# Kernel optimization log

Hardware: AMD Instinct MI355X
Metric: run time of the kernel (lower is better)

The kernel has to match this reference:

```python
import jax, jax.numpy as jnp
import numpy as np

B, N = 4, 4096
SA = 128          # SA_conv_out
DGD = 1024        # DG_conv_out
EDC = 4           # ED_conv_out
CO = 128          # conv_out
FACTOR = 0.1      # ED_radius_factor


def setup_inputs() -> dict:
    key = jax.random.key(0)
    ks = iter(jax.random.split(key, 48))
    def w(shape, s=0.02):
        return jax.random.normal(next(ks), shape, jnp.float32) * s
    def bnp(c):
        # fused inference-mode batchnorm: scale = gamma/sqrt(var+eps), shift = beta - mean*scale
        return (1.0 + jax.random.normal(next(ks), (c,), jnp.float32) * 0.05,
                jax.random.normal(next(ks), (c,), jnp.float32) * 0.05)
    xyz = jax.random.normal(next(ks), (B, N, 3), jnp.float32)
    h1 = jax.random.normal(next(ks), (B, SA, N), jnp.float32)
    h2_in = jax.random.normal(next(ks), (B, DGD, N), jnp.float32)
    dg_s1, dg_t1 = bnp(256); dg_s2, dg_t2 = bnp(64); dg_s3, dg_t3 = bnp(SA // 4)
    s1, t1 = bnp(512); s2, t2 = bnp(256); s3, t3 = bnp(CO)
    return dict(
        xyz=xyz, h1=h1, h2_in=h2_in,
        dg_w1=w((256, DGD)), dg_b1=w((256,)), dg_s1=dg_s1, dg_t1=dg_t1,
        dg_w2=w((64, 256)), dg_b2=w((64,)), dg_s2=dg_s2, dg_t2=dg_t2,
        dg_w3=w((SA // 4, 64)), dg_b3=w((SA // 4,)), dg_s3=dg_s3, dg_t3=dg_t3,
        ed_w1=w((EDC, 3), 0.3), ed_b1=w((EDC,)), ed_w2=w((EDC, EDC), 0.3), ed_b2=w((EDC,)),
        w1=w((512, SA + SA // 4 + EDC)), b1=w((512,)), s1=s1, t1=t1,
        w2=w((256, 512)), b2=w((256,)), s2=s2, t2=t2,
        w3=w((CO, 256)), b3=w((CO,)), s3=s3, t3=t3,
    )


def _conv_bn_relu(x, W, b, s, t):
    # 1x1 Conv1d + inference BN + ReLU. x: [B, Cin, N]
    y = jnp.einsum('oc,pcn->pon', W, x) + b[:, None]
    return jax.nn.relu(y * s[:, None] + t[:, None])


def _eigen_features(xyz):
    # xyz: [B, N, 3]. Adaptive-radius neighbor mask, per-point covariance, eigvalsh.
    x2 = jnp.sum(xyz * xyz, axis=-1)                                   # [B, N]
    d2 = x2[:, :, None] + x2[:, None, :] - 2.0 * jnp.einsum('pia,pja->pij', xyz, xyz)
    d = jnp.sqrt(jnp.maximum(d2, 0.0))                                 # [B, N, N]
    radius = jnp.max(d, axis=(1, 2)) * FACTOR                          # max pairwise dist per cloud
    eye = jnp.eye(N, dtype=bool)
    mask = (d < radius[:, None, None]) & ~eye                          # [B, N, N] self excluded
    wf = mask.astype(xyz.dtype)
    cnt = jnp.sum(wf, axis=-1)                                         # [B, N]
    S1 = jnp.einsum('pij,pja->pia', wf, xyz)                           # sum of neighbors
    mu = S1 / jnp.maximum(cnt, 1.0)[..., None]                         # neighbor mean
    S2 = jnp.einsum('pij,pja,pjb->piab', wf, xyz, xyz)                 # [B, N, 3, 3]
    # original divides by neighbors_mask[i].shape[0] == N (total points)
    cov = (S2 - cnt[..., None, None] * mu[..., :, None] * mu[..., None, :]) / N
    return jnp.linalg.eigvalsh(cov)                                    # [B, N, 3]


def reference(xyz, h1, h2_in,
              dg_w1, dg_b1, dg_s1, dg_t1,
              dg_w2, dg_b2, dg_s2, dg_t2,
              dg_w3, dg_b3, dg_s3, dg_t3,
              ed_w1, ed_b1, ed_w2, ed_b2,
              w1, b1, s1, t1, w2, b2, s2, t2, w3, b3, s3, t3):
    # DG feature reduction 1024 -> 256 -> 64 -> 32
    h2 = _conv_bn_relu(h2_in, dg_w1, dg_b1, dg_s1, dg_t1)
    h2 = _conv_bn_relu(h2, dg_w2, dg_b2, dg_s2, dg_t2)
    h2 = _conv_bn_relu(h2, dg_w3, dg_b3, dg_s3, dg_t3)
    # ED branch: eigenvalues of adaptive radius-neighborhood covariances
    eig = _eigen_features(xyz)                                         # [B, N, 3]
    h3 = jax.nn.relu(jnp.einsum('pni,oi->pno', eig, ed_w1) + ed_b1)
    h3 = jnp.einsum('pni,oi->pno', h3, ed_w2) + ed_b2                  # [B, N, 4]
    h3 = jnp.transpose(h3, (0, 2, 1))                                  # [B, 4, N]
    z = jnp.concatenate([h1, h2, h3], axis=1)                          # [B, 164, N]
    z = _conv_bn_relu(z, w1, b1, s1, t1)
    z = _conv_bn_relu(z, w2, b2, s2, t2)
    z = _conv_bn_relu(z, w3, b3, s3, t3)                               # [B, 128, N]
    return (xyz, z)
```

## Files before the change

### kernel.cpp

```cpp
#include <hip/hip_runtime.h>
#include <math.h>

#define N_PTS 4096
#define BATCH 4
#define JS 8
#define JCH (N_PTS / JS)

typedef short bf16x8 __attribute__((ext_vector_type(8)));
typedef short bf16x4 __attribute__((ext_vector_type(4)));
typedef float f32x4 __attribute__((ext_vector_type(4)));
typedef _Float16 f16x8 __attribute__((ext_vector_type(8)));

__device__ inline short f2h(float f) {
    _Float16 h = (_Float16)f;
    return __builtin_bit_cast(short, h);
}

__device__ inline void gload_lds16(const void* g, void* l) {
    __builtin_amdgcn_global_load_lds(
        (const __attribute__((address_space(1))) unsigned int*)g,
        (__attribute__((address_space(3))) unsigned int*)l, 16, 0, 0);
}

struct WcArgs {
    const float* W[6];
    short* O[6];
    int M[6], K[6], Kp[6];
    int start[7];
};


__device__ __forceinline__ void wconv_body(const WcArgs& a, int bx, int tid)
{
    int id = bx * 256 + tid;
    if (id >= a.start[6]) return;
    int l = 0;
    #pragma unroll
    for (int q = 1; q < 6; ++q) if (id >= a.start[q]) l = q;
    int local = id - a.start[l];
    int kp = a.Kp[l];
    int mrow = local / kp, k = local - mrow * kp;
    float v = (mrow < a.M[l] && k < a.K[l]) ? a.W[l][(size_t)mrow * a.K[l] + k] : 0.f;
    a.O[l][local] = f2h(v);
}

__device__ __forceinline__ void radius_body(
    const float* __restrict__ xyz, float* __restrict__ pmax,
    int ci, int js, int b, int tid, char* smem)
{
    if (ci >= 8 * js + 8) return;
    float4* sj = (float4*)smem;
    float* wred = (float*)(smem + JCH * 16);
    const float* xb = xyz + (size_t)b * N_PTS * 3;
    const int j0 = js * JCH;
    for (int idx = tid; idx < JCH; idx += 256) {
        int j = j0 + idx;
        float x = xb[j*3+0], y = xb[j*3+1], z = xb[j*3+2];
        sj[idx] = make_float4(x, y, z, fmaf(x, x, fmaf(y, y, z * z)));
    }
    __syncthreads();
    const int il = tid & 63;
    const int jq = tid >> 6;
    const int i = ci * 64 + il;
    const float xi = xb[i*3+0], yi = xb[i*3+1], zi = xb[i*3+2];
    const float x2i = fmaf(xi, xi, fmaf(yi, yi, zi * zi));
    float m = 0.f;
    const int jb = jq * (JCH / 4);
    #pragma unroll 4
    for (int j = jb; j < jb + JCH / 4; ++j) {
        float4 p = sj[j];
        float dot = fmaf(xi, p.x, fmaf(yi, p.y, zi * p.z));
        float d2 = fmaf(-2.f, dot, x2i + p.w);
        m = fmaxf(m, d2);
    }
    for (int off = 32; off >= 1; off >>= 1) m = fmaxf(m, __shfl_down(m, off));
    if ((tid & 63) == 0) wred[tid >> 6] = m;
    __syncthreads();
    if (tid == 0) {
        float mm = fmaxf(fmaxf(wred[0], wred[1]), fmaxf(wred[2], wred[3]));
        pmax[((size_t)b * JS + js) * 64 + ci] = mm;
    }
}

__device__ __forceinline__ void transpose_body(
    const float* __restrict__ h2, const float* __restrict__ h1,
    short* __restrict__ t_h2, short* __restrict__ zinT,
    int x, int y, int b, int tid, char* smem)
{
    float (*tile)[32] = (float(*)[32])smem;
    const int n0 = x * 32;
    const float* src = (y < 8)
        ? h2 + ((size_t)b * 1024 + y * 128) * N_PTS
        : h1 + (size_t)b * 128 * N_PTS;
    #pragma unroll
    for (int it = 0; it < 4; ++it) {
        int idx = it * 256 + tid;
        int c = idx >> 3, q = idx & 7;
        int sw = (q ^ ((c >> 3) & 7)) * 4;
        *(float4*)&tile[c][sw] = *(const float4*)&src[(size_t)c * N_PTS + n0 + q * 4];
    }
    __syncthreads();
    if (y < 8) {
        const int c0 = y * 128;
        #pragma unroll
        for (int it = 0; it < 2; ++it) {
            int idx = it * 256 + tid;
            int n = idx >> 4, cg = idx & 15;
            bf16x8 v;
            #pragma unroll
            for (int j = 0; j < 8; ++j) {
                int c = cg * 8 + j;
                v[j] = f2h(tile[c][n ^ (4 * ((c >> 3) & 7))]);
            }
            *(bf16x8*)&t_h2[((size_t)b * N_PTS + n0 + n) * 1024 + c0 + cg * 8] = v;
        }
    } else {
        #pragma unroll
        for (int it = 0; it < 2; ++it) {
            int idx = it * 256 + tid;
            int n = idx >> 4, cg = idx & 15;
            bf16x8 v;
            #pragma unroll
            for (int j = 0; j < 8; ++j) {
                int c = cg * 8 + j;
                v[j] = f2h(tile[c][n ^ (4 * ((c >> 3) & 7))]);
            }
            *(bf16x8*)&zinT[((size_t)b * N_PTS + n0 + n) * 192 + cg * 8] = v;
        }
        for (int idx = tid; idx < 32 * 7; idx += 256) {
            int n = idx / 7, cq = 164 + (idx % 7) * 4;
            bf16x4 z = {0, 0, 0, 0};
            *(bf16x4*)&zinT[((size_t)b * N_PTS + n0 + n) * 192 + cq] = z;
        }
    }
}

__device__ __forceinline__ void accum_body(
    const float* __restrict__ xyz, const float* __restrict__ pmax,
    float* __restrict__ pbuf, int ci, int js, int b, int tid, char* smem)
{
    float4* sj4 = (float4*)smem;
    _Float16 (*Ft)[JCH + 8] = (_Float16(*)[JCH + 8])(smem + 8192);
    float* redbuf = (float*)(smem + 8192 + 16 * (JCH + 8) * 2);

    const int lane = tid & 63, wave = tid >> 6;

    float mval = 0.f;
    for (int e = tid; e < 512; e += 256) {
        int js2 = e >> 6, ci2 = e & 63;
        float v = (ci2 < 8 * js2 + 8) ? pmax[((size_t)b * JS + js2) * 64 + ci2] : 0.f;
        mval = fmaxf(mval, v);
    }
    for (int off = 32; off >= 1; off >>= 1) mval = fmaxf(mval, __shfl_down(mval, off));
    if (lane == 0) redbuf[wave] = mval;

    const float* xb = xyz + (size_t)b * N_PTS * 3;
    const int j0g = js * JCH;
    for (int idx = tid; idx < JCH; idx += 256) {
        int j = j0g + idx;
        float x = xb[j*3+0], y = xb[j*3+1], z = xb[j*3+2];
        sj4[idx] = make_float4(x, y, z, fmaf(x, x, fmaf(y, y, z * z)));
        Ft[0][idx] = (_Float16)1.f;
        Ft[1][idx] = (_Float16)x;
        Ft[2][idx] = (_Float16)y;
        Ft[3][idx] = (_Float16)z;
        Ft[4][idx] = (_Float16)(x * x);
        Ft[5][idx] = (_Float16)(x * y);
        Ft[6][idx] = (_Float16)(x * z);
        Ft[7][idx] = (_Float16)(y * y);
        Ft[8][idx] = (_Float16)(y * z);
        Ft[9][idx] = (_Float16)(z * z);
        Ft[10][idx] = (_Float16)0.f; Ft[11][idx] = (_Float16)0.f;
        Ft[12][idx] = (_Float16)0.f; Ft[13][idx] = (_Float16)0.f;
        Ft[14][idx] = (_Float16)0.f; Ft[15][idx] = (_Float16)0.f;
    }
    __syncthreads();
    const float mm = fmaxf(fmaxf(redbuf[0], redbuf[1]), fmaxf(redbuf[2], redbuf[3]));
    const float r2 = 0.01f * mm;

    const int r = lane & 15, g = lane >> 4;
    const int i_wf = ci * 64 + wave * 16 + r;
    const float xi = xb[i_wf*3+0], yi = xb[i_wf*3+1], zi = xb[i_wf*3+2];
    const float x2i = fmaf(xi, xi, fmaf(yi, yi, zi * zi));

    f32x4 acc = (f32x4){0.f, 0.f, 0.f, 0.f};
    #pragma unroll 4
    for (int t = 0; t < JCH / 32; ++t) {
        const int jb = t * 32 + g * 8;
        f16x8 wfv;
        #pragma unroll
        for (int s = 0; s < 8; ++s) {
            float4 p = sj4[jb + s];
            float dot = fmaf(xi, p.x, fmaf(yi, p.y, zi * p.z));
            float d2 = fmaf(-2.f, dot, x2i + p.w);
            wfv[s] = (d2 < r2) ? (_Float16)1.f : (_Float16)0.f;
        }
        f16x8 fv = *(const f16x8*)&Ft[r][jb];
        acc = __builtin_amdgcn_mfma_f32_16x16x32_f16(wfv, fv, acc, 0, 0, 0);
    }

    const int i_out = ci * 64 + wave * 16 + g * 4;
    float* dst = pbuf + ((size_t)(b * JS + js) * N_PTS + i_out) * 16 + r;
    #pragma unroll
    for (int e = 0; e < 4; ++e) dst[(size_t)e * 16] = acc[e];
}

template<bool OUTT>
__device__ __forceinline__ void gl_body(
    const short* __restrict__ Wb, const short* __restrict__ XT,
    const float* __restrict__ bias, const float* __restrict__ scale,
    const float* __restrict__ shift, void* __restrict__ Yv,
    int M, int Kp, int ostride, size_t ybs,
    int m0, int n0, int b, int tid, char* smem)
{
    constexpr int BK = 64;
    short (*Wl)[64][BK] = (short(*)[64][BK])smem;
    short (*Xl)[64][BK] = (short(*)[64][BK])(smem + 16384);

    const int lane = tid & 63, wave = tid >> 6;
    const int g = lane >> 4, r = lane & 15;
    const int wr = wave >> 1, wc = wave & 1;
    const int wm0 = wr * 32, wn0 = wc * 32;
    const int NT = Kp / BK;

    const int lrow8 = lane >> 3;
    const int lchunk = lane & 7;

    f32x4 acc[2][2];
    #pragma unroll
    for (int i = 0; i < 2; ++i)
        #pragma unroll
        for (int j = 0; j < 2; ++j) acc[i][j] = (f32x4){0.f,0.f,0.f,0.f};

    auto stage = [&](int t, int nb) {
        #pragma unroll
        for (int i = 0; i < 2; ++i) {
            int row0 = wave * 16 + i * 8;
            int row = row0 + lrow8;
            int cl = lchunk ^ (row & 7);
            gload_lds16(&Wb[(size_t)(m0 + row) * Kp + t * BK + cl * 8],
                        &Wl[nb][row0][0]);
            gload_lds16(&XT[((size_t)b * N_PTS + n0 + row) * Kp + t * BK + cl * 8],
                        &Xl[nb][row0][0]);
        }
    };
    auto compute = [&](int cb) {
        #pragma unroll
        for (int q = 0; q < 2; ++q) {
            const int pc = ((q * 4 + g) ^ (r & 7)) * 8;
            #pragma unroll
            for (int fn = 0; fn < 2; ++fn) {
                bf16x8 bb = *(const bf16x8*)&Xl[cb][wn0 + fn * 16 + r][pc];
                #pragma unroll
                for (int fm = 0; fm < 2; ++fm) {
                    bf16x8 a = *(const bf16x8*)&Wl[cb][wm0 + fm * 16 + r][pc];
                    acc[fm][fn] = __builtin_amdgcn_mfma_f32_16x16x32_f16(
                        __builtin_bit_cast(f16x8, a),
                        __builtin_bit_cast(f16x8, bb),
                        acc[fm][fn], 0, 0, 0);
                }
            }
        }
    };

    stage(0, 0);
    __syncthreads();
    for (int t = 0; t < NT; ++t) {
        int cb = t & 1;
        if (t + 1 < NT) stage(t + 1, cb ^ 1);
        compute(cb);
        __syncthreads();
    }

    if constexpr (OUTT) {
        short* Y = (short*)Yv;
        #pragma unroll
        for (int fm = 0; fm < 2; ++fm) {
            int mb = m0 + wm0 + fm * 16 + g * 4;
            if (mb < M) {
                float4 b4 = *(const float4*)&bias[mb];
                float4 s4 = *(const float4*)&scale[mb];
                float4 h4 = *(const float4*)&shift[mb];
                #pragma unroll
                for (int fn = 0; fn < 2; ++fn) {
                    int n = n0 + wn0 + fn * 16 + r;
                    f32x4 a = acc[fm][fn];
                    bf16x4 o;
                    o[0] = f2h(fmaxf(fmaf(a[0] + b4.x, s4.x, h4.x), 0.f));
                    o[1] = f2h(fmaxf(fmaf(a[1] + b4.y, s4.y, h4.y), 0.f));
                    o[2] = f2h(fmaxf(fmaf(a[2] + b4.z, s4.z, h4.z), 0.f));
                    o[3] = f2h(fmaxf(fmaf(a[3] + b4.w, s4.w, h4.w), 0.f));
                    *(bf16x4*)&Y[((size_t)b * N_PTS + n) * ostride + mb] = o;
                }
            }
        }
    } else {
        float* Y = (float*)Yv;
        #pragma unroll
        for (int fm = 0; fm < 2; ++fm) {
            int mbase = m0 + wm0 + fm * 16 + g * 4;
            #pragma unroll
            for (int e = 0; e < 4; ++e) {
                int mm = mbase + e;
                if (mm >= M) continue;
                float bs = bias[mm], sc = scale[mm], sh = shift[mm];
                #pragma unroll
                for (int fn = 0; fn < 2; ++fn) {
                    int n = n0 + wn0 + fn * 16 + r;
                    float v = fmaxf(fmaf(acc[fm][fn][e] + bs, sc, sh), 0.f);
                    Y[(size_t)b * ybs + (size_t)mm * N_PTS + n] = v;
                }
            }
        }
    }
}

__device__ __forceinline__ void finalize_body(
    const float* __restrict__ xyz, const float* __restrict__ pbuf,
    const float* __restrict__ ew1, const float* __restrict__ eb1,
    const float* __restrict__ ew2, const float* __restrict__ eb2,
    short* __restrict__ zinT, float* __restrict__ out, int bx, int tid)
{
    int id = bx * 256 + tid;
    if (id >= BATCH * N_PTS) return;
    int b = id >> 12, i = id & (N_PTS - 1);

    out[id*3+0] = xyz[id*3+0];
    out[id*3+1] = xyz[id*3+1];
    out[id*3+2] = xyz[id*3+2];

    double s[10] = {0,0,0,0,0,0,0,0,0,0};
    for (int js = 0; js < JS; ++js) {
        const float* src = pbuf + ((size_t)(b * JS + js) * N_PTS + i) * 16;
        #pragma unroll
        for (int q = 0; q < 10; ++q) s[q] += (double)src[q];
    }
    const float* xb = xyz + (size_t)b * N_PTS * 3;
    float xi = xb[i*3+0], yi = xb[i*3+1], zi = xb[i*3+2];
    s[0] -= 1.0;
    s[1] -= (double)(float)(_Float16)xi;
    s[2] -= (double)(float)(_Float16)yi;
    s[3] -= (double)(float)(_Float16)zi;
    s[4] -= (double)(float)(_Float16)(xi * xi);
    s[5] -= (double)(float)(_Float16)(xi * yi);
    s[6] -= (double)(float)(_Float16)(xi * zi);
    s[7] -= (double)(float)(_Float16)(yi * yi);
    s[8] -= (double)(float)(_Float16)(yi * zi);
    s[9] -= (double)(float)(_Float16)(zi * zi);

    double cnt = s[0];
    double denom = fmax(cnt, 1.0);
    double mx = s[1] / denom, my = s[2] / denom, mz = s[3] / denom;
    const double invN = 1.0 / (double)N_PTS;
    double c00 = (s[4] - cnt * mx * mx) * invN;
    double c01 = (s[5] - cnt * mx * my) * invN;
    double c02 = (s[6] - cnt * mx * mz) * invN;
    double c11 = (s[7] - cnt * my * my) * invN;
    double c12 = (s[8] - cnt * my * mz) * invN;
    double c22 = (s[9] - cnt * mz * mz) * invN;

    double qm = (c00 + c11 + c22) / 3.0;
    double p1 = c01*c01 + c02*c02 + c12*c12;
    double a0 = c00 - qm, a1 = c11 - qm, a2 = c22 - qm;
    double p2 = a0*a0 + a1*a1 + a2*a2 + 2.0*p1;
    double e_lo, e_mid, e_hi;
    if (p2 < 1e-32) {
        e_lo = e_mid = e_hi = qm;
    } else {
        double p = sqrt(p2 / 6.0);
        double inv = 1.0 / p;
        double b00 = a0*inv, b11 = a1*inv, b22 = a2*inv;
        double b01 = c01*inv, b02 = c02*inv, b12 = c12*inv;
        double detB = b00*(b11*b22 - b12*b12)
                    - b01*(b01*b22 - b12*b02)
                    + b02*(b01*b12 - b11*b02);
        double r = 0.5 * detB;
        r = fmin(1.0, fmax(-1.0, r));
        double phi = acos(r) / 3.0;
        double two_p = 2.0 * p;
        e_hi = qm + two_p * cos(phi);
        e_lo = qm + two_p * cos(phi + 2.0943951023931953);
        e_mid = 3.0 * qm - e_hi - e_lo;
    }
    float e0 = (float)e_lo, e1 = (float)e_mid, e2 = (float)e_hi;

    float t[4];
    #pragma unroll
    for (int o = 0; o < 4; ++o)
        t[o] = fmaxf(e0 * ew1[o*3+0] + e1 * ew1[o*3+1] +
                     e2 * ew1[o*3+2] + eb1[o], 0.f);
    bf16x4 ov;
    #pragma unroll
    for (int o = 0; o < 4; ++o) {
        float h = t[0]*ew2[o*4+0] + t[1]*ew2[o*4+1] +
                  t[2]*ew2[o*4+2] + t[3]*ew2[o*4+3] + eb2[o];
        ov[o] = f2h(h);
    }
    *(bf16x4*)&zinT[((size_t)b * N_PTS + i) * 192 + 160] = ov;
}

__device__ __forceinline__ void dg23_body(
    const short* __restrict__ W2b, const short* __restrict__ W3b,
    const short* __restrict__ XT,
    const float* __restrict__ cb2, const float* __restrict__ cs2,
    const float* __restrict__ ct2,
    const float* __restrict__ cb3, const float* __restrict__ cs3,
    const float* __restrict__ ct3,
    short* __restrict__ zinT, int x, int b, int tid, char* smem)
{
    constexpr int BK = 64;
    short (*Wl)[64][64] = (short(*)[64][64])smem;
    short (*Xl)[64][64] = (short(*)[64][64])(smem + 16384);
    short (*Wl3)[72] = (short(*)[72])(smem + 32768);
    short (*Xl3)[72] = (short(*)[72])(smem + 32768 + 9216);

    const int lane = tid & 63, wave = tid >> 6;
    const int g = lane >> 4, r = lane & 15;
    const int wr = wave >> 1, wc = wave & 1;
    const int wm0 = wr * 32, wn0 = wc * 32;
    const int n0 = x * 64;
    const int Kp = 256, NT = 4;

    const int lrow8 = lane >> 3;
    const int lchunk = lane & 7;

    #pragma unroll
    for (int u = 0; u < 2; ++u) {
        int id = u * 256 + tid;
        int m = id >> 3, c = id & 7;
        *(bf16x8*)&Wl3[m][c * 8] = *(const bf16x8*)&W3b[(size_t)m * 64 + c * 8];
    }

    f32x4 acc[2][2];
    #pragma unroll
    for (int i = 0; i < 2; ++i)
        #pragma unroll
        for (int j = 0; j < 2; ++j) acc[i][j] = (f32x4){0.f,0.f,0.f,0.f};

    auto stage = [&](int t, int nb) {
        #pragma unroll
        for (int i = 0; i < 2; ++i) {
            int row0 = wave * 16 + i * 8;
            int row = row0 + lrow8;
            int cl = lchunk ^ (row & 7);
            gload_lds16(&W2b[(size_t)row * Kp + t * BK + cl * 8],
                        &Wl[nb][row0][0]);
            gload_lds16(&XT[((size_t)b * N_PTS + n0 + row) * Kp + t * BK + cl * 8],
                        &Xl[nb][row0][0]);
        }
    };
    auto compute = [&](int cb) {
        #pragma unroll
        for (int q = 0; q < 2; ++q) {
            const int pc = ((q * 4 + g) ^ (r & 7)) * 8;
            #pragma unroll
            for (int fn = 0; fn < 2; ++fn) {
                bf16x8 bb = *(const bf16x8*)&Xl[cb][wn0 + fn * 16 + r][pc];
                #pragma unroll
                for (int fm = 0; fm < 2; ++fm) {
                    bf16x8 a = *(const bf16x8*)&Wl[cb][wm0 + fm * 16 + r][pc];
                    acc[fm][fn] = __builtin_amdgcn_mfma_f32_16x16x32_f16(
                        __builtin_bit_cast(f16x8, a),
                        __builtin_bit_cast(f16x8, bb),
                        acc[fm][fn], 0, 0, 0);
                }
            }
        }
    };

    stage(0, 0);
    __syncthreads();
    for (int t = 0; t < NT; ++t) {
        int cb = t & 1;
        if (t + 1 < NT) stage(t + 1, cb ^ 1);
        compute(cb);
        __syncthreads();
    }

    #pragma unroll
    for (int fm = 0; fm < 2; ++fm) {
        int mb = wm0 + fm * 16 + g * 4;
        float4 b4 = *(const float4*)&cb2[mb];
        float4 s4 = *(const float4*)&cs2[mb];
        float4 h4 = *(const float4*)&ct2[mb];
        #pragma unroll
        for (int fn = 0; fn < 2; ++fn) {
            int nl = wn0 + fn * 16 + r;
            f32x4 a = acc[fm][fn];
            bf16x4 o;
            o[0] = f2h(fmaxf(fmaf(a[0] + b4.x, s4.x, h4.x), 0.f));
            o[1] = f2h(fmaxf(fmaf(a[1] + b4.y, s4.y, h4.y), 0.f));
            o[2] = f2h(fmaxf(fmaf(a[2] + b4.z, s4.z, h4.z), 0.f));
            o[3] = f2h(fmaxf(fmaf(a[3] + b4.w, s4.w, h4.w), 0.f));
            *(bf16x4*)&Xl3[nl][mb] = o;
        }
    }
    __syncthreads();

    f32x4 acc3[2][2];
    #pragma unroll
    for (int i = 0; i < 2; ++i)
        #pragma unroll
        for (int j = 0; j < 2; ++j) acc3[i][j] = (f32x4){0.f,0.f,0.f,0.f};
    #pragma unroll
    for (int q = 0; q < 2; ++q) {
        #pragma unroll
        for (int fn = 0; fn < 2; ++fn) {
            bf16x8 bb = *(const bf16x8*)&Xl3[wn0 + fn * 16 + r][q * 32 + g * 8];
            #pragma unroll
            for (int fm = 0; fm < 2; ++fm) {
                bf16x8 a = *(const bf16x8*)&Wl3[wm0 + fm * 16 + r][q * 32 + g * 8];
                acc3[fm][fn] = __builtin_amdgcn_mfma_f32_16x16x32_f16(
                    __builtin_bit_cast(f16x8, a),
                    __builtin_bit_cast(f16x8, bb),
                    acc3[fm][fn], 0, 0, 0);
            }
        }
    }

    #pragma unroll
    for (int fm = 0; fm < 2; ++fm) {
        int mb = wm0 + fm * 16 + g * 4;
        if (mb < 32) {
            float4 b4 = *(const float4*)&cb3[mb];
            float4 s4 = *(const float4*)&cs3[mb];
            float4 h4 = *(const float4*)&ct3[mb];
            #pragma unroll
            for (int fn = 0; fn < 2; ++fn) {
                int n = n0 + wn0 + fn * 16 + r;
                f32x4 a = acc3[fm][fn];
                bf16x4 o;
                o[0] = f2h(fmaxf(fmaf(a[0] + b4.x, s4.x, h4.x), 0.f));
                o[1] = f2h(fmaxf(fmaf(a[1] + b4.y, s4.y, h4.y), 0.f));
                o[2] = f2h(fmaxf(fmaf(a[2] + b4.z, s4.z, h4.z), 0.f));
                o[3] = f2h(fmaxf(fmaf(a[3] + b4.w, s4.w, h4.w), 0.f));
                *(bf16x4*)&zinT[((size_t)b * N_PTS + n) * 192 + 128 + mb] = o;
            }
        }
    }
}


__global__ __launch_bounds__(256) void megaA_kernel(
    WcArgs wa, int wcBlocks,
    const float* __restrict__ xyz, float* __restrict__ pmax,
    const float* __restrict__ h2, const float* __restrict__ h1,
    short* __restrict__ t_h2, short* __restrict__ zinT)
{
    __shared__ __align__(16) char smem[16896];
    const int tid = threadIdx.x;
    int bx = blockIdx.x;
    if (bx < wcBlocks) { wconv_body(wa, bx, tid); return; }
    bx -= wcBlocks;
    if (bx < 2048) {
        int ci = bx & 63, js = (bx >> 6) & 7, b = bx >> 9;
        radius_body(xyz, pmax, ci, js, b, tid, smem);
        return;
    }
    bx -= 2048;
    int x = bx & 127, rest = bx >> 7;
    int y = rest % 9, b = rest / 9;
    transpose_body(h2, h1, t_h2, zinT, x, y, b, tid, smem);
}

__global__ __launch_bounds__(256) void megaB_kernel(
    const float* __restrict__ xyz, const float* __restrict__ pmax,
    float* __restrict__ pbuf,
    const short* __restrict__ wb1, const short* __restrict__ t_h2,
    const float* __restrict__ db1, const float* __restrict__ ds1,
    const float* __restrict__ dt1, short* __restrict__ bufA)
{
    __shared__ __align__(16) char smem[32768];
    const int tid = threadIdx.x;
    int bx = blockIdx.x;
    if (bx < 2048) {
        int ci = bx & 63, js = (bx >> 6) & 7, b = bx >> 9;
        accum_body(xyz, pmax, pbuf, ci, js, b, tid, smem);
    } else {
        int e = bx - 2048;
        int x = e & 63, my = (e >> 6) & 3, b = e >> 8;
        gl_body<true>(wb1, t_h2, db1, ds1, dt1, bufA,
                      256, 1024, 256, 0, my * 64, x * 64, b, tid, smem);
    }
}

__global__ __launch_bounds__(256) void megaC_kernel(
    const float* __restrict__ xyz, const float* __restrict__ pbuf,
    const float* __restrict__ ew1, const float* __restrict__ eb1,
    const float* __restrict__ ew2, const float* __restrict__ eb2,
    float* __restrict__ out,
    const short* __restrict__ wb2, const short* __restrict__ wb3,
    const short* __restrict__ bufA,
    const float* __restrict__ cb2, const float* __restrict__ cs2,
    const float* __restrict__ ct2,
    const float* __restrict__ cb3, const float* __restrict__ cs3,
    const float* __restrict__ ct3,
    short* __restrict__ zinT)
{
    __shared__ __align__(16) char smem[51200];
    const int tid = threadIdx.x;
    int bx = blockIdx.x;
    if (bx < 64) {
        finalize_body(xyz, pbuf, ew1, eb1, ew2, eb2, zinT, out, bx, tid);
    } else {
        int e = bx - 64;
        int x = e & 63, b = e >> 6;
        dg23_body(wb2, wb3, bufA, cb2, cs2, ct2, cb3, cs3, ct3,
                  zinT, x, b, tid, smem);
    }
}

template<bool OUTT>
__global__ __launch_bounds__(256) void mfma_gemm_gl(
    const short* __restrict__ Wb, const short* __restrict__ XT,
    const float* __restrict__ bias, const float* __restrict__ scale,
    const float* __restrict__ shift, void* __restrict__ Yv,
    int M, int Kp, int ostride, size_t ybs)
{
    __shared__ __align__(16) char smem[32768];
    gl_body<OUTT>(Wb, XT, bias, scale, shift, Yv, M, Kp, ostride, ybs,
                  blockIdx.y * 64, blockIdx.x * 64, blockIdx.z,
                  threadIdx.x, smem);
}

extern "C" void kernel_launch(void* const* d_in, const int* in_sizes, int n_in,
                              void* d_out, int out_size, void* d_ws, size_t ws_size,
                              hipStream_t stream)
{
    const float* xyz   = (const float*)d_in[0];
    const float* h1    = (const float*)d_in[1];
    const float* h2_in = (const float*)d_in[2];
    const float* dg_w1 = (const float*)d_in[3];
    const float* dg_b1 = (const float*)d_in[4];
    const float* dg_s1 = (const float*)d_in[5];
    const float* dg_t1 = (const float*)d_in[6];
    const float* dg_w2 = (const float*)d_in[7];
    const float* dg_b2 = (const float*)d_in[8];
    const float* dg_s2 = (const float*)d_in[9];
    const float* dg_t2 = (const float*)d_in[10];
    const float* dg_w3 = (const float*)d_in[11];
    const float* dg_b3 = (const float*)d_in[12];
    const float* dg_s3 = (const float*)d_in[13];
    const float* dg_t3 = (const float*)d_in[14];
    const float* ed_w1 = (const float*)d_in[15];
    const float* ed_b1 = (const float*)d_in[16];
    const float* ed_w2 = (const float*)d_in[17];
    const float* ed_b2 = (const float*)d_in[18];
    const float* w1 = (const float*)d_in[19];
    const float* b1 = (const float*)d_in[20];
    const float* s1 = (const float*)d_in[21];
    const float* t1 = (const float*)d_in[22];
    const float* w2 = (const float*)d_in[23];
    const float* b2 = (const float*)d_in[24];
    const float* s2 = (const float*)d_in[25];
    const float* t2 = (const float*)d_in[26];
    const float* w3 = (const float*)d_in[27];
    const float* b3 = (const float*)d_in[28];
    const float* s3 = (const float*)d_in[29];
    const float* t3 = (const float*)d_in[30];

    float* out = (float*)d_out;

    char* ws = (char*)d_ws;
    size_t off = 0;
    auto alloc = [&](size_t bytes) {
        char* p = ws + off;
        off += (bytes + 255) & ~(size_t)255;
        return p;
    };
    float* pmax = (float*)alloc((size_t)BATCH * JS * 64 * 4);
    short* wb1  = (short*)alloc((size_t)256 * 1024 * 2);
    short* wb2  = (short*)alloc((size_t)64  * 256  * 2);
    short* wb3  = (short*)alloc((size_t)64  * 64   * 2);
    short* wbf1 = (short*)alloc((size_t)512 * 192  * 2);
    short* wbf2 = (short*)alloc((size_t)256 * 512  * 2);
    short* wbf3 = (short*)alloc((size_t)128 * 256  * 2);
    short* zinT = (short*)alloc((size_t)BATCH * N_PTS * 192 * 2);
    short* t_h2 = (short*)alloc((size_t)BATCH * N_PTS * 1024 * 2);
    short* bufA = (short*)alloc((size_t)BATCH * N_PTS * 256 * 2);
    float* pbuf = (float*)alloc((size_t)BATCH * JS * N_PTS * 16 * 4);
    short* bufB = t_h2;
    short* bufD = bufA;

    WcArgs wa;
    int wcTotal;
    {
        const float* Wp[6] = {dg_w1, dg_w2, dg_w3, w1, w2, w3};
        short* Op[6] = {wb1, wb2, wb3, wbf1, wbf2, wbf3};
        int Mv[6] = {256, 64, 32, 512, 256, 128};
        int Kv[6] = {1024, 256, 64, 164, 512, 256};
        int Mp[6] = {256, 64, 64, 512, 256, 128};
        int Kp[6] = {1024, 256, 64, 192, 512, 256};
        int acc0 = 0;
        for (int l = 0; l < 6; ++l) {
            wa.W[l] = Wp[l]; wa.O[l] = Op[l];
            wa.M[l] = Mv[l]; wa.K[l] = Kv[l]; wa.Kp[l] = Kp[l];
            wa.start[l] = acc0;
            acc0 += Mp[l] * Kp[l];
        }
        wa.start[6] = acc0;
        wcTotal = acc0;
    }
    const int wcBlocks = (wcTotal + 255) / 256;

    {
        int grid = wcBlocks + 2048 + 128 * 9 * BATCH;
        megaA_kernel<<<grid, 256, 0, stream>>>(
            wa, wcBlocks, xyz, pmax, h2_in, h1, t_h2, zinT);
    }
    megaB_kernel<<<2048 + 64 * 4 * BATCH, 256, 0, stream>>>(
        xyz, pmax, pbuf, wb1, t_h2, dg_b1, dg_s1, dg_t1, bufA);
    megaC_kernel<<<64 + 64 * BATCH, 256, 0, stream>>>(
        xyz, pbuf, ed_w1, ed_b1, ed_w2, ed_b2, out,
        wb2, wb3, bufA, dg_b2, dg_s2, dg_t2, dg_b3, dg_s3, dg_t3, zinT);

    mfma_gemm_gl<true><<<dim3(N_PTS/64, 8, BATCH), 256, 0, stream>>>(
        wbf1, zinT, b1, s1, t1, bufB, 512, 192, 512, 0);
    mfma_gemm_gl<true><<<dim3(N_PTS/64, 4, BATCH), 256, 0, stream>>>(
        wbf2, bufB, b2, s2, t2, bufD, 256, 512, 256, 0);
    mfma_gemm_gl<false><<<dim3(N_PTS/64, 2, BATCH), 256, 0, stream>>>(
        wbf3, bufD, b3, s3, t3, out + (size_t)BATCH * N_PTS * 3, 128, 256, 0,
        (size_t)128 * N_PTS);
}
```

Before: 100.7 us.

## Widen transpose tiles, reorder megaA blocks, add 128x64 GEMM for first fused conv

Transpose blocks now handle 64 points instead of 32, halving their count, and are dispatched first in megaA. The weight-conversion blocks are moved to the end of the grid. A new 128x64-tile MFMA GEMM replaces the 64x64 one for the 512x192 first conv layer, so each X tile is reused across more output rows. In exchange, shared memory grows to 48 KB in the GEMM and 32 KB in megaA, which may reduce occupancy.

```diff
diff --git a/kernel.cpp b/kernel.cpp
--- a/kernel.cpp
+++ b/kernel.cpp
@@ -82,52 +82,54 @@
     }
 }
 
-__device__ __forceinline__ void transpose_body(
+__device__ __forceinline__ void transpose64_body(
     const float* __restrict__ h2, const float* __restrict__ h1,
     short* __restrict__ t_h2, short* __restrict__ zinT,
     int x, int y, int b, int tid, char* smem)
 {
-    float (*tile)[32] = (float(*)[32])smem;
-    const int n0 = x * 32;
+    float (*tile)[64] = (float(*)[64])smem;
+    const int n0 = x * 64;
     const float* src = (y < 8)
         ? h2 + ((size_t)b * 1024 + y * 128) * N_PTS
         : h1 + (size_t)b * 128 * N_PTS;
     #pragma unroll
-    for (int it = 0; it < 4; ++it) {
+    for (int it = 0; it < 8; ++it) {
         int idx = it * 256 + tid;
-        int c = idx >> 3, q = idx & 7;
-        int sw = (q ^ ((c >> 3) & 7)) * 4;
-        *(float4*)&tile[c][sw] = *(const float4*)&src[(size_t)c * N_PTS + n0 + q * 4];
+        int c = idx >> 4, q = idx & 15;
+        int qs = q ^ ((c >> 3) & 7);
+        *(float4*)&tile[c][qs * 4] = *(const float4*)&src[(size_t)c * N_PTS + n0 + q * 4];
     }
     __syncthreads();
     if (y < 8) {
         const int c0 = y * 128;
         #pragma unroll
-        for (int it = 0; it < 2; ++it) {
+        for (int it = 0; it < 4; ++it) {
             int idx = it * 256 + tid;
             int n = idx >> 4, cg = idx & 15;
             bf16x8 v;
             #pragma unroll
             for (int j = 0; j < 8; ++j) {
                 int c = cg * 8 + j;
-                v[j] = f2h(tile[c][n ^ (4 * ((c >> 3) & 7))]);
+                int col = (((n >> 2) ^ ((c >> 3) & 7)) << 2) | (n & 3);
+                v[j] = f2h(tile[c][col]);
             }
             *(bf16x8*)&t_h2[((size_t)b * N_PTS + n0 + n) * 1024 + c0 + cg * 8] = v;
         }
     } else {
         #pragma unroll
-        for (int it = 0; it < 2; ++it) {
+        for (int it = 0; it < 4; ++it) {
             int idx = it * 256 + tid;
             int n = idx >> 4, cg = idx & 15;
             bf16x8 v;
             #pragma unroll
             for (int j = 0; j < 8; ++j) {
                 int c = cg * 8 + j;
-                v[j] = f2h(tile[c][n ^ (4 * ((c >> 3) & 7))]);
+                int col = (((n >> 2) ^ ((c >> 3) & 7)) << 2) | (n & 3);
+                v[j] = f2h(tile[c][col]);
             }
             *(bf16x8*)&zinT[((size_t)b * N_PTS + n0 + n) * 192 + cg * 8] = v;
         }
-        for (int idx = tid; idx < 32 * 7; idx += 256) {
+        for (int idx = tid; idx < 64 * 7; idx += 256) {
             int n = idx / 7, cq = 164 + (idx % 7) * 4;
             bf16x4 z = {0, 0, 0, 0};
             *(bf16x4*)&zinT[((size_t)b * N_PTS + n0 + n) * 192 + cq] = z;
@@ -310,6 +312,100 @@
                     float v = fmaxf(fmaf(acc[fm][fn][e] + bs, sc, sh), 0.f);
                     Y[(size_t)b * ybs + (size_t)mm * N_PTS + n] = v;
                 }
+            }
+        }
+    }
+}
+
+__device__ __forceinline__ void gl128_body(
+    const short* __restrict__ Wb, const short* __restrict__ XT,
+    const float* __restrict__ bias, const float* __restrict__ scale,
+    const float* __restrict__ shift, short* __restrict__ Y,
+    int M, int Kp, int ostride,
+    int m0, int n0, int b, int tid, char* smem)
+{
+    constexpr int BK = 64;
+    short (*Wl)[128][BK] = (short(*)[128][BK])smem;
+    short (*Xl)[64][BK] = (short(*)[64][BK])(smem + 32768);
+
+    const int lane = tid & 63, wave = tid >> 6;
+    const int g = lane >> 4, r = lane & 15;
+    const int wr = wave >> 1, wc = wave & 1;
+    const int wm0 = wr * 64, wn0 = wc * 32;
+    const int NT = Kp / BK;
+
+    const int lrow8 = lane >> 3;
+    const int lchunk = lane & 7;
+
+    f32x4 acc[4][2];
+    #pragma unroll
+    for (int i = 0; i < 4; ++i)
+        #pragma unroll
+        for (int j = 0; j < 2; ++j) acc[i][j] = (f32x4){0.f,0.f,0.f,0.f};
+
+    auto stage = [&](int t, int nb) {
+        #pragma unroll
+        for (int i = 0; i < 4; ++i) {
+            int row0 = wave * 32 + i * 8;
+            int row = row0 + lrow8;
+            int cl = lchunk ^ (row & 7);
+            gload_lds16(&Wb[(size_t)(m0 + row) * Kp + t * BK + cl * 8],
+                        &Wl[nb][row0][0]);
+        }
+        #pragma unroll
+        for (int i = 0; i < 2; ++i) {
+            int row0 = wave * 16 + i * 8;
+            int row = row0 + lrow8;
+            int cl = lchunk ^ (row & 7);
+            gload_lds16(&XT[((size_t)b * N_PTS + n0 + row) * Kp + t * BK + cl * 8],
+                        &Xl[nb][row0][0]);
+        }
+    };
+    auto compute = [&](int cb) {
+        #pragma unroll
+        for (int q = 0; q < 2; ++q) {
+            const int pc = ((q * 4 + g) ^ (r & 7)) * 8;
+            #pragma unroll
+            for (int fn = 0; fn < 2; ++fn) {
+                bf16x8 bb = *(const bf16x8*)&Xl[cb][wn0 + fn * 16 + r][pc];
+                #pragma unroll
+                for (int fm = 0; fm < 4; ++fm) {
+                    bf16x8 a = *(const bf16x8*)&Wl[cb][wm0 + fm * 16 + r][pc];
+                    acc[fm][fn] = __builtin_amdgcn_mfma_f32_16x16x32_f16(
+                        __builtin_bit_cast(f16x8, a),
+                        __builtin_bit_cast(f16x8, bb),
+                        acc[fm][fn], 0, 0, 0);
+                }
+            }
+        }
+    };
+
+    stage(0, 0);
+    __syncthreads();
+    for (int t = 0; t < NT; ++t) {
+        int cb = t & 1;
+        if (t + 1 < NT) stage(t + 1, cb ^ 1);
+        compute(cb);
+        __syncthreads();
+    }
+
+    #pragma unroll
+    for (int fm = 0; fm < 4; ++fm) {
+        int mb = m0 + wm0 + fm * 16 + g * 4;
+        if (mb < M) {
+            float4 b4 = *(const float4*)&bias[mb];
+            float4 s4 = *(const float4*)&scale[mb];
+            float4 h4 = *(const float4*)&shift[mb];
+            #pragma unroll
+            for (int fn = 0; fn < 2; ++fn) {
+                int n = n0 + wn0 + fn * 16 + r;
+                f32x4 a = acc[fm][fn];
+                bf16x4 o;
+                o[0] = f2h(fmaxf(fmaf(a[0] + b4.x, s4.x, h4.x), 0.f));
+                o[1] = f2h(fmaxf(fmaf(a[1] + b4.y, s4.y, h4.y), 0.f));
+                o[2] = f2h(fmaxf(fmaf(a[2] + b4.z, s4.z, h4.z), 0.f));
+                o[3] = f2h(fmaxf(fmaf(a[3] + b4.w, s4.w, h4.w), 0.f));
+                *(bf16x4*)&Y[((size_t)b * N_PTS + n) * ostride + mb] = o;
             }
         }
     }
@@ -542,25 +638,29 @@
 
 
 __global__ __launch_bounds__(256) void megaA_kernel(
-    WcArgs wa, int wcBlocks,
+    WcArgs wa,
     const float* __restrict__ xyz, float* __restrict__ pmax,
     const float* __restrict__ h2, const float* __restrict__ h1,
     short* __restrict__ t_h2, short* __restrict__ zinT)
 {
-    __shared__ __align__(16) char smem[16896];
+    __shared__ __align__(16) char smem[32768];
     const int tid = threadIdx.x;
     int bx = blockIdx.x;
-    if (bx < wcBlocks) { wconv_body(wa, bx, tid); return; }
-    bx -= wcBlocks;
+    const int nTrans = 64 * 9 * BATCH;
+    if (bx < nTrans) {
+        int x = bx & 63, rest = bx >> 6;
+        int y = rest % 9, b = rest / 9;
+        transpose64_body(h2, h1, t_h2, zinT, x, y, b, tid, smem);
+        return;
+    }
+    bx -= nTrans;
     if (bx < 2048) {
         int ci = bx & 63, js = (bx >> 6) & 7, b = bx >> 9;
         radius_body(xyz, pmax, ci, js, b, tid, smem);
         return;
     }
     bx -= 2048;
-    int x = bx & 127, rest = bx >> 7;
-    int y = rest % 9, b = rest / 9;
-    transpose_body(h2, h1, t_h2, zinT, x, y, b, tid, smem);
+    wconv_body(wa, bx, tid);
 }
 
 __global__ __launch_bounds__(256) void megaB_kernel(
@@ -621,6 +721,18 @@
     gl_body<OUTT>(Wb, XT, bias, scale, shift, Yv, M, Kp, ostride, ybs,
                   blockIdx.y * 64, blockIdx.x * 64, blockIdx.z,
                   threadIdx.x, smem);
+}
+
+__global__ __launch_bounds__(256) void mfma_gemm_gl128(
+    const short* __restrict__ Wb, const short* __restrict__ XT,
+    const float* __restrict__ bias, const float* __restrict__ scale,
+    const float* __restrict__ shift, short* __restrict__ Y,
+    int M, int Kp, int ostride)
+{
+    __shared__ __align__(16) char smem[49152];
+    gl128_body(Wb, XT, bias, scale, shift, Y, M, Kp, ostride,
+               blockIdx.y * 128, blockIdx.x * 64, blockIdx.z,
+               threadIdx.x, smem);
 }
 
 extern "C" void kernel_launch(void* const* d_in, const int* in_sizes, int n_in,
@@ -704,9 +816,9 @@
     const int wcBlocks = (wcTotal + 255) / 256;
 
     {
-        int grid = wcBlocks + 2048 + 128 * 9 * BATCH;
+        int grid = 64 * 9 * BATCH + 2048 + wcBlocks;
         megaA_kernel<<<grid, 256, 0, stream>>>(
-            wa, wcBlocks, xyz, pmax, h2_in, h1, t_h2, zinT);
+            wa, xyz, pmax, h2_in, h1, t_h2, zinT);
     }
     megaB_kernel<<<2048 + 64 * 4 * BATCH, 256, 0, stream>>>(
         xyz, pmax, pbuf, wb1, t_h2, dg_b1, dg_s1, dg_t1, bufA);
@@ -714,8 +826,8 @@
         xyz, pbuf, ed_w1, ed_b1, ed_w2, ed_b2, out,
         wb2, wb3, bufA, dg_b2, dg_s2, dg_t2, dg_b3, dg_s3, dg_t3, zinT);
 
-    mfma_gemm_gl<true><<<dim3(N_PTS/64, 8, BATCH), 256, 0, stream>>>(
-        wbf1, zinT, b1, s1, t1, bufB, 512, 192, 512, 0);
+    mfma_gemm_gl128<<<dim3(N_PTS/64, 4, BATCH), 256, 0, stream>>>(
+        wbf1, zinT, b1, s1, t1, bufB, 512, 192, 512);
     mfma_gemm_gl<true><<<dim3(N_PTS/64, 4, BATCH), 256, 0, stream>>>(
         wbf2, bufB, b2, s2, t2, bufD, 256, 512, 256, 0);
     mfma_gemm_gl<false><<<dim3(N_PTS/64, 2, BATCH), 256, 0, stream>>>(
```

New measurement: 110.2 us. +9.5%, slower.
